# Kernel optimization log

Measured on AMD Instinct MI355X. Metric: run time of the kernel, lower is better.

Reference implementation:

```python
import jax, jax.numpy as jnp
import numpy as np

N_NODES = 100000
N_EDGES = 1600000
IN_SIZE = 128
HIDDEN = 128
OUT_SIZE = 64


def setup_inputs() -> dict:
    key = jax.random.key(0)
    k = jax.random.split(key, 8)
    feat = jax.random.normal(k[0], (N_NODES, IN_SIZE), dtype=jnp.float32)
    src = jax.random.randint(k[1], (N_EDGES,), 0, N_NODES, dtype=jnp.int32)
    dst = jax.random.randint(k[2], (N_EDGES,), 0, N_NODES, dtype=jnp.int32)
    # fc_neigh weights for the two SAGEConv layers (stored as [in, out])
    W1 = jax.random.normal(k[3], (IN_SIZE, HIDDEN), dtype=jnp.float32) / np.sqrt(IN_SIZE)
    b1 = jnp.zeros((HIDDEN,), dtype=jnp.float32)
    W2 = jax.random.normal(k[4], (HIDDEN, OUT_SIZE), dtype=jnp.float32) / np.sqrt(HIDDEN)
    b2 = jnp.zeros((OUT_SIZE,), dtype=jnp.float32)
    return {"feat": feat, "W1": W1, "b1": b1, "W2": W2, "b2": b2,
            "src": src, "dst": dst}


def _sage_gcn(h, src, dst, W, b):
    # DGL SAGEConv with aggregator_type='gcn':
    #   neigh = segment_sum over incoming edges of src features
    #   h_neigh = (neigh + h_self) / (in_degree + 1)
    #   out = h_neigh @ W + b   (fc_self is not used for 'gcn')
    neigh = jax.ops.segment_sum(h[src], dst, num_segments=N_NODES)  # [N, d]
    deg = jax.ops.segment_sum(jnp.ones((src.shape[0],), dtype=h.dtype), dst,
                              num_segments=N_NODES)                 # [N]
    h_neigh = (neigh + h) / (deg + 1.0)[:, None]
    return h_neigh @ W + b


def reference(feat, W1, b1, W2, b2, src, dst):
    # dropout(p=0.0) is identity; activation between layers only
    h = _sage_gcn(feat, src, dst, W1, b1)
    h = jax.nn.relu(h)
    h = _sage_gcn(h, src, dst, W2, b2)
    return h
```

## Files before the change

kernel.cpp:

```cpp
#include <hip/hip_runtime.h>

#define NNODES 100000
#define NEDGES 1600000
#define NB 391
#define BSHIFT 8

typedef _Float16 f16;
typedef _Float16 v4h __attribute__((ext_vector_type(4)));
typedef _Float16 v8h __attribute__((ext_vector_type(8)));
typedef float v4f __attribute__((ext_vector_type(4)));

__global__ void cvt_w_both(const float* __restrict__ W1, f16* __restrict__ W1t,
                           const float* __restrict__ W2, f16* __restrict__ W2t) {
    int t = blockIdx.x * blockDim.x + threadIdx.x;
    if (t < 128 * 128) {
        int k = t >> 7, n = t & 127;
        W1t[n * 128 + k] = (f16)W1[k * 128 + n];
    } else if (t < 128 * 128 + 128 * 64) {
        int u = t - 128 * 128;
        int k = u >> 6, n = u & 63;
        W2t[n * 128 + k] = (f16)W2[k * 64 + n];
    }
}

__global__ __launch_bounds__(256) void bucket_hist(const int* __restrict__ dst,
                                                   int* __restrict__ bhist) {
    __shared__ int h[NB];
    for (int i = threadIdx.x; i < NB; i += 256) h[i] = 0;
    __syncthreads();
    int base = blockIdx.x * 4096;
    for (int k = 0; k < 16; k++) {
        int e = base + k * 256 + threadIdx.x;
        if (e < NEDGES) atomicAdd(&h[dst[e] >> BSHIFT], 1);
    }
    __syncthreads();
    for (int i = threadIdx.x; i < NB; i += 256)
        if (h[i]) atomicAdd(&bhist[i], h[i]);
}

__global__ void bucket_scan(const int* __restrict__ bhist, int* __restrict__ boff,
                            int* __restrict__ bcur) {
    __shared__ int s[512];
    int tid = threadIdx.x;
    int v = (tid < NB) ? bhist[tid] : 0;
    s[tid] = v;
    __syncthreads();
    for (int off = 1; off < 512; off <<= 1) {
        int t = (tid >= off) ? s[tid - off] : 0;
        __syncthreads();
        s[tid] += t;
        __syncthreads();
    }
    int excl = s[tid] - v;
    if (tid < NB) { boff[tid] = excl; bcur[tid] = excl; }
    if (tid == NB - 1) boff[NB] = excl + v;
}

__global__ __launch_bounds__(256) void bucket_scatter(const int* __restrict__ src,
                                                      const int* __restrict__ dst,
                                                      int* __restrict__ bcur,
                                                      int* __restrict__ ebuf) {
    __shared__ int h[NB];
    __shared__ int base_s[NB];
    for (int i = threadIdx.x; i < NB; i += 256) h[i] = 0;
    __syncthreads();
    int base = blockIdx.x * 4096;
    int d[16], sv[16];
    for (int k = 0; k < 16; k++) {
        int e = base + k * 256 + threadIdx.x;
        if (e < NEDGES) {
            d[k] = dst[e];
            sv[k] = src[e];
            atomicAdd(&h[d[k] >> BSHIFT], 1);
        } else {
            d[k] = -1;
        }
    }
    __syncthreads();
    for (int i = threadIdx.x; i < NB; i += 256) {
        int c = h[i];
        if (c) base_s[i] = atomicAdd(&bcur[i], c);
        h[i] = 0;
    }
    __syncthreads();
    for (int k = 0; k < 16; k++) {
        if (d[k] >= 0) {
            int b = d[k] >> BSHIFT;
            int slot = atomicAdd(&h[b], 1);
            ebuf[base_s[b] + slot] = sv[k] | ((d[k] & 255) << 24);
        }
    }
}

__global__ __launch_bounds__(256) void fill_bucket(const int* __restrict__ ebuf,
                                                   const int* __restrict__ boff,
                                                   int* __restrict__ offs,
                                                   int* __restrict__ csr) {
    __shared__ int lc[256];
    __shared__ int ls[256];
    int b = blockIdx.x;
    int tid = threadIdx.x;
    lc[tid] = 0;
    __syncthreads();
    int ebeg = boff[b], eend = boff[b + 1];
    for (int e = ebeg + tid; e < eend; e += 256)
        atomicAdd(&lc[((unsigned)ebuf[e]) >> 24], 1);
    __syncthreads();
    int cnt = lc[tid];
    ls[tid] = cnt;
    __syncthreads();
    for (int off = 1; off < 256; off <<= 1) {
        int t = (tid >= off) ? ls[tid - off] : 0;
        __syncthreads();
        ls[tid] += t;
        __syncthreads();
    }
    int excl = ls[tid] - cnt;
    int nb = b << BSHIFT;
    int node = nb + tid;
    if (node < NNODES) offs[node] = ebeg + excl;
    if (node == NNODES - 1) offs[NNODES] = NEDGES;
    ls[tid] = excl;
    lc[tid] = 0;
    __syncthreads();
    for (int e = ebeg + tid; e < eend; e += 256) {
        int p = ebuf[e];
        int dloc = ((unsigned)p) >> 24;
        int slot = atomicAdd(&lc[dloc], 1);
        csr[ebeg + ls[dloc] + slot] = p & 0xFFFFFF;
    }
}

template <int NOUT>
__global__ __launch_bounds__(256) void gemm_mfma(
    const f16* __restrict__ A, const f16* __restrict__ Wt, f16* __restrict__ out) {
    constexpr int PITCH = 136;
    __shared__ f16 wlds[NOUT * PITCH];
    int tid = threadIdx.x;
    for (int c = tid; c < NOUT * 16; c += 256) {
        int n = c >> 4;
        int kc = c & 15;
        *(v8h*)&wlds[n * PITCH + kc * 8] = *(const v8h*)&Wt[n * 128 + kc * 8];
    }
    __syncthreads();

    int wave = tid >> 6, lane = tid & 63, quad = lane >> 4, l16 = lane & 15;
    int m0 = blockIdx.x * 64 + wave * 16;
    if (m0 >= NNODES) return;

    v8h a[4];
    const f16* arow = A + (long)(m0 + l16) * 128 + quad * 8;
#pragma unroll
    for (int kb = 0; kb < 4; kb++) a[kb] = *(const v8h*)(arow + kb * 32);

#pragma unroll
    for (int nt = 0; nt < NOUT / 16; nt++) {
        v4f acc = {0.f, 0.f, 0.f, 0.f};
        const f16* brow = &wlds[(nt * 16 + l16) * PITCH + quad * 8];
#pragma unroll
        for (int kb = 0; kb < 4; kb++) {
            v8h b = *(const v8h*)(brow + kb * 32);
            acc = __builtin_amdgcn_mfma_f32_16x16x32_f16(a[kb], b, acc, 0, 0, 0);
        }
        int n = nt * 16 + l16;
#pragma unroll
        for (int r = 0; r < 4; r++)
            out[(long)(m0 + quad * 4 + r) * NOUT + n] = (f16)acc[r];
    }
}

template <int NOUT>
__global__ __launch_bounds__(256) void gemm_mfma_f32in(
    const float* __restrict__ A, const f16* __restrict__ Wt, f16* __restrict__ out) {
    constexpr int PITCH = 136;
    __shared__ f16 wlds[NOUT * PITCH];
    int tid = threadIdx.x;
    for (int c = tid; c < NOUT * 16; c += 256) {
        int n = c >> 4;
        int kc = c & 15;
        *(v8h*)&wlds[n * PITCH + kc * 8] = *(const v8h*)&Wt[n * 128 + kc * 8];
    }
    __syncthreads();

    int wave = tid >> 6, lane = tid & 63, quad = lane >> 4, l16 = lane & 15;
    int m0 = blockIdx.x * 64 + wave * 16;
    if (m0 >= NNODES) return;

    v8h a[4];
    const float* arow = A + (long)(m0 + l16) * 128 + quad * 8;
#pragma unroll
    for (int kb = 0; kb < 4; kb++) {
        float4 f0 = *(const float4*)(arow + kb * 32);
        float4 f1 = *(const float4*)(arow + kb * 32 + 4);
        v8h t = {(f16)f0.x, (f16)f0.y, (f16)f0.z, (f16)f0.w,
                 (f16)f1.x, (f16)f1.y, (f16)f1.z, (f16)f1.w};
        a[kb] = t;
    }

#pragma unroll
    for (int nt = 0; nt < NOUT / 16; nt++) {
        v4f acc = {0.f, 0.f, 0.f, 0.f};
        const f16* brow = &wlds[(nt * 16 + l16) * PITCH + quad * 8];
#pragma unroll
        for (int kb = 0; kb < 4; kb++) {
            v8h b = *(const v8h*)(brow + kb * 32);
            acc = __builtin_amdgcn_mfma_f32_16x16x32_f16(a[kb], b, acc, 0, 0, 0);
        }
        int n = nt * 16 + l16;
#pragma unroll
        for (int r = 0; r < 4; r++)
            out[(long)(m0 + quad * 4 + r) * NOUT + n] = (f16)acc[r];
    }
}

__global__ void gather128(const v4h* __restrict__ z, const int* __restrict__ offs,
                          const int* __restrict__ csr, const float* __restrict__ bias,
                          v4h* __restrict__ out) {
    int node = (int)(((long)blockIdx.x * blockDim.x + threadIdx.x) >> 6);
    if (node >= NNODES) return;
    int lane = threadIdx.x & 63;
    int half = lane >> 5;
    int c = lane & 31;

    int beg = offs[node];
    int end = offs[node + 1];
    float a0 = 0.f, a1 = 0.f, a2 = 0.f, a3 = 0.f;

    int e = beg;
    for (; e + 7 < end; e += 8) {
        int i0 = csr[e + half];
        int i1 = csr[e + 2 + half];
        int i2 = csr[e + 4 + half];
        int i3 = csr[e + 6 + half];
        v4h u0 = z[(long)i0 * 32 + c];
        v4h u1 = z[(long)i1 * 32 + c];
        v4h u2 = z[(long)i2 * 32 + c];
        v4h u3 = z[(long)i3 * 32 + c];
        a0 += (float)u0[0] + (float)u1[0] + (float)u2[0] + (float)u3[0];
        a1 += (float)u0[1] + (float)u1[1] + (float)u2[1] + (float)u3[1];
        a2 += (float)u0[2] + (float)u1[2] + (float)u2[2] + (float)u3[2];
        a3 += (float)u0[3] + (float)u1[3] + (float)u2[3] + (float)u3[3];
    }
    for (; e + 3 < end; e += 4) {
        int i0 = csr[e + half];
        int i1 = csr[e + 2 + half];
        v4h u0 = z[(long)i0 * 32 + c];
        v4h u1 = z[(long)i1 * 32 + c];
        a0 += (float)u0[0] + (float)u1[0];
        a1 += (float)u0[1] + (float)u1[1];
        a2 += (float)u0[2] + (float)u1[2];
        a3 += (float)u0[3] + (float)u1[3];
    }
    for (; e < end; e += 2) {
        int t = e + half;
        if (t < end) {
            v4h u = z[(long)csr[t] * 32 + c];
            a0 += (float)u[0]; a1 += (float)u[1];
            a2 += (float)u[2]; a3 += (float)u[3];
        }
    }
    if (half == 0) {
        v4h s = z[(long)node * 32 + c];
        a0 += (float)s[0]; a1 += (float)s[1];
        a2 += (float)s[2]; a3 += (float)s[3];
    }
    a0 += __shfl_xor(a0, 32);
    a1 += __shfl_xor(a1, 32);
    a2 += __shfl_xor(a2, 32);
    a3 += __shfl_xor(a3, 32);

    if (half == 0) {
        float inv = 1.0f / (float)(end - beg + 1);
        float4 b = ((const float4*)bias)[c];
        v4h o = {(f16)fmaxf(a0 * inv + b.x, 0.f),
                 (f16)fmaxf(a1 * inv + b.y, 0.f),
                 (f16)fmaxf(a2 * inv + b.z, 0.f),
                 (f16)fmaxf(a3 * inv + b.w, 0.f)};
        out[(long)node * 32 + c] = o;
    }
}

__global__ void gather64(const v4h* __restrict__ z, const int* __restrict__ offs,
                         const int* __restrict__ csr, const float* __restrict__ bias,
                         float4* __restrict__ out) {
    int node = (int)(((long)blockIdx.x * blockDim.x + threadIdx.x) >> 6);
    if (node >= NNODES) return;
    int lane = threadIdx.x & 63;
    int sub = lane >> 4;
    int c = lane & 15;

    int beg = offs[node];
    int end = offs[node + 1];
    float a0 = 0.f, a1 = 0.f, a2 = 0.f, a3 = 0.f;

    int e = beg;
    for (; e + 15 < end; e += 16) {
        int i0 = csr[e + sub];
        int i1 = csr[e + 4 + sub];
        int i2 = csr[e + 8 + sub];
        int i3 = csr[e + 12 + sub];
        v4h u0 = z[(long)i0 * 16 + c];
        v4h u1 = z[(long)i1 * 16 + c];
        v4h u2 = z[(long)i2 * 16 + c];
        v4h u3 = z[(long)i3 * 16 + c];
        a0 += (float)u0[0] + (float)u1[0] + (float)u2[0] + (float)u3[0];
        a1 += (float)u0[1] + (float)u1[1] + (float)u2[1] + (float)u3[1];
        a2 += (float)u0[2] + (float)u1[2] + (float)u2[2] + (float)u3[2];
        a3 += (float)u0[3] + (float)u1[3] + (float)u2[3] + (float)u3[3];
    }
    for (; e + 7 < end; e += 8) {
        int i0 = csr[e + sub];
        int i1 = csr[e + 4 + sub];
        v4h u0 = z[(long)i0 * 16 + c];
        v4h u1 = z[(long)i1 * 16 + c];
        a0 += (float)u0[0] + (float)u1[0];
        a1 += (float)u0[1] + (float)u1[1];
        a2 += (float)u0[2] + (float)u1[2];
        a3 += (float)u0[3] + (float)u1[3];
    }
    for (; e < end; e += 4) {
        int t = e + sub;
        if (t < end) {
            v4h u = z[(long)csr[t] * 16 + c];
            a0 += (float)u[0]; a1 += (float)u[1];
            a2 += (float)u[2]; a3 += (float)u[3];
        }
    }
    if (sub == 0) {
        v4h s = z[(long)node * 16 + c];
        a0 += (float)s[0]; a1 += (float)s[1];
        a2 += (float)s[2]; a3 += (float)s[3];
    }
    a0 += __shfl_xor(a0, 16);  a0 += __shfl_xor(a0, 32);
    a1 += __shfl_xor(a1, 16);  a1 += __shfl_xor(a1, 32);
    a2 += __shfl_xor(a2, 16);  a2 += __shfl_xor(a2, 32);
    a3 += __shfl_xor(a3, 16);  a3 += __shfl_xor(a3, 32);

    if (sub == 0) {
        float inv = 1.0f / (float)(end - beg + 1);
        float4 b = ((const float4*)bias)[c];
        out[(long)node * 16 + c] =
            make_float4(a0 * inv + b.x, a1 * inv + b.y, a2 * inv + b.z, a3 * inv + b.w);
    }
}

extern "C" void kernel_launch(void* const* d_in, const int* in_sizes, int n_in,
                              void* d_out, int out_size, void* d_ws, size_t ws_size,
                              hipStream_t stream) {
    const float* feat = (const float*)d_in[0];
    const float* W1   = (const float*)d_in[1];
    const float* b1   = (const float*)d_in[2];
    const float* W2   = (const float*)d_in[3];
    const float* b2   = (const float*)d_in[4];
    const int*   src  = (const int*)d_in[5];
    const int*   dst  = (const int*)d_in[6];
    float* out = (float*)d_out;

    char* ws = (char*)d_ws;
    int* bhist = (int*)(ws + 0x0000000);
    int* boff  = (int*)(ws + 0x0001000);
    int* bcur  = (int*)(ws + 0x0002000);
    int* offs  = (int*)(ws + 0x0003000);
    int* csr   = (int*)(ws + 0x0070000);
    int* ebuf  = (int*)(ws + 0x0700000);
    f16* z1    = (f16*)(ws + 0x0E00000);
    f16* h1    = (f16*)(ws + 0x2700000);
    f16* z2    = (f16*)(ws + 0x4000000);
    f16* W1t   = (f16*)(ws + 0x4D00000);
    f16* W2t   = (f16*)(ws + 0x4D10000);

    cvt_w_both<<<(128 * 128 + 128 * 64 + 255) / 256, 256, 0, stream>>>(W1, W1t, W2, W2t);

    hipMemsetAsync(bhist, 0, NB * sizeof(int), stream);
    const int EBLOCKS = (NEDGES + 4095) / 4096;
    bucket_hist<<<EBLOCKS, 256, 0, stream>>>(dst, bhist);
    bucket_scan<<<1, 512, 0, stream>>>(bhist, boff, bcur);
    bucket_scatter<<<EBLOCKS, 256, 0, stream>>>(src, dst, bcur, ebuf);
    fill_bucket<<<NB, 256, 0, stream>>>(ebuf, boff, offs, csr);

    const int GATHER_BLOCKS = (NNODES * 64 + 255) / 256;
    const int GEMM_BLOCKS = (NNODES + 63) / 64;

    gemm_mfma_f32in<128><<<GEMM_BLOCKS, 256, 0, stream>>>(feat, W1t, z1);
    gather128<<<GATHER_BLOCKS, 256, 0, stream>>>((const v4h*)z1, offs, csr, b1,
                                                 (v4h*)h1);

    gemm_mfma<64><<<GEMM_BLOCKS, 256, 0, stream>>>(h1, W2t, z2);
    gather64<<<GATHER_BLOCKS, 256, 0, stream>>>((const v4h*)z2, offs, csr, b2,
                                                (float4*)out);
}
```

Measured before the change: 292.3 us.

## Merge independent kernels into shared launches and deepen gather unrolling with fp16 partial sums

The weight conversion now shares a launch with the bucket histogram, and the layer-1 GEMM shares a launch with the bucket scatter through block-index branching. This removes two kernel launches and lets independent work overlap on the GPU. The gather kernels now process 8 neighbors per iteration, sum them pairwise in fp16 before converting to fp32, and load the self feature early. The fp16 partial sums lose precision, and the merged GEMM blocks need more LDS, which may limit occupancy for the scatter blocks.

```diff
diff --git a/kernel.cpp b/kernel.cpp
--- a/kernel.cpp
+++ b/kernel.cpp
@@ -4,28 +4,34 @@
 #define NEDGES 1600000
 #define NB 391
 #define BSHIFT 8
+#define EBLOCKS 391
+#define GEMM_BLOCKS 1563
+#define CVT_BLOCKS 96
 
 typedef _Float16 f16;
 typedef _Float16 v4h __attribute__((ext_vector_type(4)));
 typedef _Float16 v8h __attribute__((ext_vector_type(8)));
 typedef float v4f __attribute__((ext_vector_type(4)));
 
-__global__ void cvt_w_both(const float* __restrict__ W1, f16* __restrict__ W1t,
-                           const float* __restrict__ W2, f16* __restrict__ W2t) {
-    int t = blockIdx.x * blockDim.x + threadIdx.x;
-    if (t < 128 * 128) {
-        int k = t >> 7, n = t & 127;
-        W1t[n * 128 + k] = (f16)W1[k * 128 + n];
-    } else if (t < 128 * 128 + 128 * 64) {
-        int u = t - 128 * 128;
-        int k = u >> 6, n = u & 63;
-        W2t[n * 128 + k] = (f16)W2[k * 64 + n];
-    }
-}
-
-__global__ __launch_bounds__(256) void bucket_hist(const int* __restrict__ dst,
-                                                   int* __restrict__ bhist) {
+__global__ __launch_bounds__(256) void hist_cvt(const int* __restrict__ dst,
+                                                int* __restrict__ bhist,
+                                                const float* __restrict__ W1,
+                                                f16* __restrict__ W1t,
+                                                const float* __restrict__ W2,
+                                                f16* __restrict__ W2t) {
     __shared__ int h[NB];
+    if (blockIdx.x >= EBLOCKS) {
+        int t = (blockIdx.x - EBLOCKS) * 256 + threadIdx.x;
+        if (t < 128 * 128) {
+            int k = t >> 7, n = t & 127;
+            W1t[n * 128 + k] = (f16)W1[k * 128 + n];
+        } else if (t < 128 * 128 + 128 * 64) {
+            int u = t - 128 * 128;
+            int k = u >> 6, n = u & 63;
+            W2t[n * 128 + k] = (f16)W2[k * 64 + n];
+        }
+        return;
+    }
     for (int i = threadIdx.x; i < NB; i += 256) h[i] = 0;
     __syncthreads();
     int base = blockIdx.x * 4096;
@@ -56,39 +62,85 @@
     if (tid == NB - 1) boff[NB] = excl + v;
 }
 
-__global__ __launch_bounds__(256) void bucket_scatter(const int* __restrict__ src,
-                                                      const int* __restrict__ dst,
-                                                      int* __restrict__ bcur,
-                                                      int* __restrict__ ebuf) {
-    __shared__ int h[NB];
-    __shared__ int base_s[NB];
-    for (int i = threadIdx.x; i < NB; i += 256) h[i] = 0;
-    __syncthreads();
-    int base = blockIdx.x * 4096;
-    int d[16], sv[16];
-    for (int k = 0; k < 16; k++) {
-        int e = base + k * 256 + threadIdx.x;
-        if (e < NEDGES) {
-            d[k] = dst[e];
-            sv[k] = src[e];
-            atomicAdd(&h[d[k] >> BSHIFT], 1);
-        } else {
-            d[k] = -1;
-        }
-    }
-    __syncthreads();
-    for (int i = threadIdx.x; i < NB; i += 256) {
-        int c = h[i];
-        if (c) base_s[i] = atomicAdd(&bcur[i], c);
-        h[i] = 0;
-    }
-    __syncthreads();
-    for (int k = 0; k < 16; k++) {
-        if (d[k] >= 0) {
-            int b = d[k] >> BSHIFT;
-            int slot = atomicAdd(&h[b], 1);
-            ebuf[base_s[b] + slot] = sv[k] | ((d[k] & 255) << 24);
-        }
+__global__ __launch_bounds__(256) void scatter_gemm1(
+    const int* __restrict__ src, const int* __restrict__ dst,
+    int* __restrict__ bcur, int* __restrict__ ebuf,
+    const float* __restrict__ feat, const f16* __restrict__ W1t,
+    f16* __restrict__ z1) {
+    constexpr int PITCH = 136;
+    __shared__ __align__(16) char smem[128 * PITCH * 2];
+    int tid = threadIdx.x;
+
+    if (blockIdx.x < EBLOCKS) {
+        int* h = (int*)smem;
+        int* base_s = ((int*)smem) + 512;
+        for (int i = tid; i < NB; i += 256) h[i] = 0;
+        __syncthreads();
+        int base = blockIdx.x * 4096;
+        int d[16], sv[16];
+        for (int k = 0; k < 16; k++) {
+            int e = base + k * 256 + tid;
+            if (e < NEDGES) {
+                d[k] = dst[e];
+                sv[k] = src[e];
+                atomicAdd(&h[d[k] >> BSHIFT], 1);
+            } else {
+                d[k] = -1;
+            }
+        }
+        __syncthreads();
+        for (int i = tid; i < NB; i += 256) {
+            int c = h[i];
+            if (c) base_s[i] = atomicAdd(&bcur[i], c);
+            h[i] = 0;
+        }
+        __syncthreads();
+        for (int k = 0; k < 16; k++) {
+            if (d[k] >= 0) {
+                int b = d[k] >> BSHIFT;
+                int slot = atomicAdd(&h[b], 1);
+                ebuf[base_s[b] + slot] = sv[k] | ((d[k] & 255) << 24);
+            }
+        }
+        return;
+    }
+
+    f16* wlds = (f16*)smem;
+    for (int c = tid; c < 128 * 16; c += 256) {
+        int n = c >> 4;
+        int kc = c & 15;
+        *(v8h*)&wlds[n * PITCH + kc * 8] = *(const v8h*)&W1t[n * 128 + kc * 8];
+    }
+    __syncthreads();
+
+    int wave = tid >> 6, lane = tid & 63, quad = lane >> 4, l16 = lane & 15;
+    int m0 = (blockIdx.x - EBLOCKS) * 64 + wave * 16;
+    if (m0 >= NNODES) return;
+
+    v8h a[4];
+    const float* arow = feat + (long)(m0 + l16) * 128 + quad * 8;
+#pragma unroll
+    for (int kb = 0; kb < 4; kb++) {
+        float4 f0 = *(const float4*)(arow + kb * 32);
+        float4 f1 = *(const float4*)(arow + kb * 32 + 4);
+        v8h t = {(f16)f0.x, (f16)f0.y, (f16)f0.z, (f16)f0.w,
+                 (f16)f1.x, (f16)f1.y, (f16)f1.z, (f16)f1.w};
+        a[kb] = t;
+    }
+
+#pragma unroll
+    for (int nt = 0; nt < 8; nt++) {
+        v4f acc = {0.f, 0.f, 0.f, 0.f};
+        const f16* brow = &wlds[(nt * 16 + l16) * PITCH + quad * 8];
+#pragma unroll
+        for (int kb = 0; kb < 4; kb++) {
+            v8h b = *(const v8h*)(brow + kb * 32);
+            acc = __builtin_amdgcn_mfma_f32_16x16x32_f16(a[kb], b, acc, 0, 0, 0);
+        }
+        int n = nt * 16 + l16;
+#pragma unroll
+        for (int r = 0; r < 4; r++)
+            z1[(long)(m0 + quad * 4 + r) * 128 + n] = (f16)acc[r];
     }
 }
 
@@ -116,8 +168,7 @@
         __syncthreads();
     }
     int excl = ls[tid] - cnt;
-    int nb = b << BSHIFT;
-    int node = nb + tid;
+    int node = (b << BSHIFT) + tid;
     if (node < NNODES) offs[node] = ebeg + excl;
     if (node == NNODES - 1) offs[NNODES] = NEDGES;
     ls[tid] = excl;
@@ -131,13 +182,13 @@
     }
 }
 
-template <int NOUT>
-__global__ __launch_bounds__(256) void gemm_mfma(
-    const f16* __restrict__ A, const f16* __restrict__ Wt, f16* __restrict__ out) {
+__global__ __launch_bounds__(256) void gemm2(const f16* __restrict__ A,
+                                             const f16* __restrict__ Wt,
+                                             f16* __restrict__ out) {
     constexpr int PITCH = 136;
-    __shared__ f16 wlds[NOUT * PITCH];
+    __shared__ f16 wlds[64 * PITCH];
     int tid = threadIdx.x;
-    for (int c = tid; c < NOUT * 16; c += 256) {
+    for (int c = tid; c < 64 * 16; c += 256) {
         int n = c >> 4;
         int kc = c & 15;
         *(v8h*)&wlds[n * PITCH + kc * 8] = *(const v8h*)&Wt[n * 128 + kc * 8];
@@ -154,7 +205,7 @@
     for (int kb = 0; kb < 4; kb++) a[kb] = *(const v8h*)(arow + kb * 32);
 
 #pragma unroll
-    for (int nt = 0; nt < NOUT / 16; nt++) {
+    for (int nt = 0; nt < 4; nt++) {
         v4f acc = {0.f, 0.f, 0.f, 0.f};
         const f16* brow = &wlds[(nt * 16 + l16) * PITCH + quad * 8];
 #pragma unroll
@@ -165,51 +216,7 @@
         int n = nt * 16 + l16;
 #pragma unroll
         for (int r = 0; r < 4; r++)
-            out[(long)(m0 + quad * 4 + r) * NOUT + n] = (f16)acc[r];
-    }
-}
-
-template <int NOUT>
-__global__ __launch_bounds__(256) void gemm_mfma_f32in(
-    const float* __restrict__ A, const f16* __restrict__ Wt, f16* __restrict__ out) {
-    constexpr int PITCH = 136;
-    __shared__ f16 wlds[NOUT * PITCH];
-    int tid = threadIdx.x;
-    for (int c = tid; c < NOUT * 16; c += 256) {
-        int n = c >> 4;
-        int kc = c & 15;
-        *(v8h*)&wlds[n * PITCH + kc * 8] = *(const v8h*)&Wt[n * 128 + kc * 8];
-    }
-    __syncthreads();
-
-    int wave = tid >> 6, lane = tid & 63, quad = lane >> 4, l16 = lane & 15;
-    int m0 = blockIdx.x * 64 + wave * 16;
-    if (m0 >= NNODES) return;
-
-    v8h a[4];
-    const float* arow = A + (long)(m0 + l16) * 128 + quad * 8;
-#pragma unroll
-    for (int kb = 0; kb < 4; kb++) {
-        float4 f0 = *(const float4*)(arow + kb * 32);
-        float4 f1 = *(const float4*)(arow + kb * 32 + 4);
-        v8h t = {(f16)f0.x, (f16)f0.y, (f16)f0.z, (f16)f0.w,
-                 (f16)f1.x, (f16)f1.y, (f16)f1.z, (f16)f1.w};
-        a[kb] = t;
-    }
-
-#pragma unroll
-    for (int nt = 0; nt < NOUT / 16; nt++) {
-        v4f acc = {0.f, 0.f, 0.f, 0.f};
-        const f16* brow = &wlds[(nt * 16 + l16) * PITCH + quad * 8];
-#pragma unroll
-        for (int kb = 0; kb < 4; kb++) {
-            v8h b = *(const v8h*)(brow + kb * 32);
-            acc = __builtin_amdgcn_mfma_f32_16x16x32_f16(a[kb], b, acc, 0, 0, 0);
-        }
-        int n = nt * 16 + l16;
-#pragma unroll
-        for (int r = 0; r < 4; r++)
-            out[(long)(m0 + quad * 4 + r) * NOUT + n] = (f16)acc[r];
+            out[(long)(m0 + quad * 4 + r) * 64 + n] = (f16)acc[r];
     }
 }
 
@@ -224,32 +231,44 @@
 
     int beg = offs[node];
     int end = offs[node + 1];
+
+    v4h sv = {0, 0, 0, 0};
+    if (half == 0) sv = z[(long)node * 32 + c];
+
     float a0 = 0.f, a1 = 0.f, a2 = 0.f, a3 = 0.f;
 
     int e = beg;
-    for (; e + 7 < end; e += 8) {
+    for (; e + 15 < end; e += 16) {
         int i0 = csr[e + half];
         int i1 = csr[e + 2 + half];
         int i2 = csr[e + 4 + half];
         int i3 = csr[e + 6 + half];
+        int i4 = csr[e + 8 + half];
+        int i5 = csr[e + 10 + half];
+        int i6 = csr[e + 12 + half];
+        int i7 = csr[e + 14 + half];
         v4h u0 = z[(long)i0 * 32 + c];
         v4h u1 = z[(long)i1 * 32 + c];
         v4h u2 = z[(long)i2 * 32 + c];
         v4h u3 = z[(long)i3 * 32 + c];
-        a0 += (float)u0[0] + (float)u1[0] + (float)u2[0] + (float)u3[0];
-        a1 += (float)u0[1] + (float)u1[1] + (float)u2[1] + (float)u3[1];
-        a2 += (float)u0[2] + (float)u1[2] + (float)u2[2] + (float)u3[2];
-        a3 += (float)u0[3] + (float)u1[3] + (float)u2[3] + (float)u3[3];
+        v4h u4 = z[(long)i4 * 32 + c];
+        v4h u5 = z[(long)i5 * 32 + c];
+        v4h u6 = z[(long)i6 * 32 + c];
+        v4h u7 = z[(long)i7 * 32 + c];
+        v4h s01 = u0 + u1, s23 = u2 + u3, s45 = u4 + u5, s67 = u6 + u7;
+        v4h s03 = s01 + s23, s47 = s45 + s67;
+        v4h s = s03 + s47;
+        a0 += (float)s[0]; a1 += (float)s[1];
+        a2 += (float)s[2]; a3 += (float)s[3];
     }
     for (; e + 3 < end; e += 4) {
         int i0 = csr[e + half];
         int i1 = csr[e + 2 + half];
         v4h u0 = z[(long)i0 * 32 + c];
         v4h u1 = z[(long)i1 * 32 + c];
-        a0 += (float)u0[0] + (float)u1[0];
-        a1 += (float)u0[1] + (float)u1[1];
-        a2 += (float)u0[2] + (float)u1[2];
-        a3 += (float)u0[3] + (float)u1[3];
+        v4h s = u0 + u1;
+        a0 += (float)s[0]; a1 += (float)s[1];
+        a2 += (float)s[2]; a3 += (float)s[3];
     }
     for (; e < end; e += 2) {
         int t = e + half;
@@ -259,11 +278,9 @@
             a2 += (float)u[2]; a3 += (float)u[3];
         }
     }
-    if (half == 0) {
-        v4h s = z[(long)node * 32 + c];
-        a0 += (float)s[0]; a1 += (float)s[1];
-        a2 += (float)s[2]; a3 += (float)s[3];
-    }
+    a0 += (float)sv[0]; a1 += (float)sv[1];
+    a2 += (float)sv[2]; a3 += (float)sv[3];
+
     a0 += __shfl_xor(a0, 32);
     a1 += __shfl_xor(a1, 32);
     a2 += __shfl_xor(a2, 32);
@@ -291,32 +308,44 @@
 
     int beg = offs[node];
     int end = offs[node + 1];
+
+    v4h sv = {0, 0, 0, 0};
+    if (sub == 0) sv = z[(long)node * 16 + c];
+
     float a0 = 0.f, a1 = 0.f, a2 = 0.f, a3 = 0.f;
 
     int e = beg;
-    for (; e + 15 < end; e += 16) {
+    for (; e + 31 < end; e += 32) {
         int i0 = csr[e + sub];
         int i1 = csr[e + 4 + sub];
         int i2 = csr[e + 8 + sub];
         int i3 = csr[e + 12 + sub];
+        int i4 = csr[e + 16 + sub];
+        int i5 = csr[e + 20 + sub];
+        int i6 = csr[e + 24 + sub];
+        int i7 = csr[e + 28 + sub];
         v4h u0 = z[(long)i0 * 16 + c];
         v4h u1 = z[(long)i1 * 16 + c];
         v4h u2 = z[(long)i2 * 16 + c];
         v4h u3 = z[(long)i3 * 16 + c];
-        a0 += (float)u0[0] + (float)u1[0] + (float)u2[0] + (float)u3[0];
-        a1 += (float)u0[1] + (float)u1[1] + (float)u2[1] + (float)u3[1];
-        a2 += (float)u0[2] + (float)u1[2] + (float)u2[2] + (float)u3[2];
-        a3 += (float)u0[3] + (float)u1[3] + (float)u2[3] + (float)u3[3];
+        v4h u4 = z[(long)i4 * 16 + c];
+        v4h u5 = z[(long)i5 * 16 + c];
+        v4h u6 = z[(long)i6 * 16 + c];
+        v4h u7 = z[(long)i7 * 16 + c];
+        v4h s01 = u0 + u1, s23 = u2 + u3, s45 = u4 + u5, s67 = u6 + u7;
+        v4h s03 = s01 + s23, s47 = s45 + s67;
+        v4h s = s03 + s47;
+        a0 += (float)s[0]; a1 += (float)s[1];
+        a2 += (float)s[2]; a3 += (float)s[3];
     }
     for (; e + 7 < end; e += 8) {
         int i0 = csr[e + sub];
         int i1 = csr[e + 4 + sub];
         v4h u0 = z[(long)i0 * 16 + c];
         v4h u1 = z[(long)i1 * 16 + c];
-        a0 += (float)u0[0] + (float)u1[0];
-        a1 += (float)u0[1] + (float)u1[1];
-        a2 += (float)u0[2] + (float)u1[2];
-        a3 += (float)u0[3] + (float)u1[3];
+        v4h s = u0 + u1;
+        a0 += (float)s[0]; a1 += (float)s[1];
+        a2 += (float)s[2]; a3 += (float)s[3];
     }
     for (; e < end; e += 4) {
         int t = e + sub;
@@ -326,11 +355,9 @@
             a2 += (float)u[2]; a3 += (float)u[3];
         }
     }
-    if (sub == 0) {
-        v4h s = z[(long)node * 16 + c];
-        a0 += (float)s[0]; a1 += (float)s[1];
-        a2 += (float)s[2]; a3 += (float)s[3];
-    }
+    a0 += (float)sv[0]; a1 += (float)sv[1];
+    a2 += (float)sv[2]; a3 += (float)sv[3];
+
     a0 += __shfl_xor(a0, 16);  a0 += __shfl_xor(a0, 32);
     a1 += __shfl_xor(a1, 16);  a1 += __shfl_xor(a1, 32);
     a2 += __shfl_xor(a2, 16);  a2 += __shfl_xor(a2, 32);
@@ -369,23 +396,20 @@
     f16* W1t   = (f16*)(ws + 0x4D00000);
     f16* W2t   = (f16*)(ws + 0x4D10000);
 
-    cvt_w_both<<<(128 * 128 + 128 * 64 + 255) / 256, 256, 0, stream>>>(W1, W1t, W2, W2t);
-
     hipMemsetAsync(bhist, 0, NB * sizeof(int), stream);
-    const int EBLOCKS = (NEDGES + 4095) / 4096;
-    bucket_hist<<<EBLOCKS, 256, 0, stream>>>(dst, bhist);
+
+    hist_cvt<<<EBLOCKS + CVT_BLOCKS, 256, 0, stream>>>(dst, bhist, W1, W1t, W2, W2t);
     bucket_scan<<<1, 512, 0, stream>>>(bhist, boff, bcur);
-    bucket_scatter<<<EBLOCKS, 256, 0, stream>>>(src, dst, bcur, ebuf);
+
+    scatter_gemm1<<<EBLOCKS + GEMM_BLOCKS, 256, 0, stream>>>(src, dst, bcur, ebuf,
+                                                             feat, W1t, z1);
     fill_bucket<<<NB, 256, 0, stream>>>(ebuf, boff, offs, csr);
 
     const int GATHER_BLOCKS = (NNODES * 64 + 255) / 256;
-    const int GEMM_BLOCKS = (NNODES + 63) / 64;
-
-    gemm_mfma_f32in<128><<<GEMM_BLOCKS, 256, 0, stream>>>(feat, W1t, z1);
+
     gather128<<<GATHER_BLOCKS, 256, 0, stream>>>((const v4h*)z1, offs, csr, b1,
                                                  (v4h*)h1);
-
-    gemm_mfma<64><<<GEMM_BLOCKS, 256, 0, stream>>>(h1, W2t, z2);
+    gemm2<<<GEMM_BLOCKS, 256, 0, stream>>>(h1, W2t, z2);
     gather64<<<GATHER_BLOCKS, 256, 0, stream>>>((const v4h*)z2, offs, csr, b2,
                                                 (float4*)out);
 }
```

Result: faster. 278.3 us (-4.8%).
